# Performance work log

Measured on AMD Instinct MI355X. Metric: run time of the kernel, lower is better.

The kernel has to match this reference:

```python
import jax, jax.numpy as jnp
import numpy as np

N = 20000      # nodes
E = 320000     # edges (avg in-degree 16)
R = 100        # relation types
F = 256        # in_ent_feats == out_ent_feats == in_rel_feats
H = 8          # heads
D = F // H     # head dim = 32
HOP = 5        # PPR hops
ALPHA = 0.1
SLOPE = 0.2    # LeakyReLU negative slope


def _ln(x, g, b, eps=1e-5):
    m = x.mean(-1, keepdims=True)
    v = ((x - m) ** 2).mean(-1, keepdims=True)
    return (x - m) / jnp.sqrt(v + eps) * g + b


def setup_inputs() -> dict:
    key = jax.random.key(0)
    ks = jax.random.split(key, 12)
    s = 1.0 / np.sqrt(F)
    ent_feat = jax.random.normal(ks[0], (N, F), jnp.float32)
    rel_feat = jax.random.normal(ks[1], (R, F), jnp.float32)
    W_head = jax.random.normal(ks[2], (F, F), jnp.float32) * s
    W_tail = jax.random.normal(ks[3], (F, F), jnp.float32) * s
    W_ent = jax.random.normal(ks[4], (F, F), jnp.float32) * s
    W_rel = jax.random.normal(ks[5], (F, F), jnp.float32) * s
    attn = jax.random.normal(ks[6], (1, H, D), jnp.float32) * s
    ln_ent_g = jnp.ones((F,), jnp.float32); ln_ent_b = jnp.zeros((F,), jnp.float32)
    ln_rel_g = jnp.ones((F,), jnp.float32); ln_rel_b = jnp.zeros((F,), jnp.float32)
    ln_ff_g = jnp.ones((F,), jnp.float32); ln_ff_b = jnp.zeros((F,), jnp.float32)
    W1 = jax.random.normal(ks[7], (F, 4 * F), jnp.float32) * s
    b1 = jnp.zeros((4 * F,), jnp.float32)
    W2 = jax.random.normal(ks[8], (4 * F, F), jnp.float32) * (0.5 * s)
    b2 = jnp.zeros((F,), jnp.float32)
    src = jax.random.randint(ks[9], (E,), 0, N, dtype=jnp.int32)
    # every node must have in-degree >= 1 (DGL raises on 0-in-degree nodes)
    dst = jnp.concatenate([jnp.arange(N, dtype=jnp.int32),
                           jax.random.randint(ks[10], (E - N,), 0, N, dtype=jnp.int32)])
    rid = jax.random.randint(ks[11], (E,), 0, R, dtype=jnp.int32)
    return {"ent_feat": ent_feat, "rel_feat": rel_feat,
            "W_head": W_head, "W_tail": W_tail, "W_ent": W_ent, "W_rel": W_rel,
            "attn": attn,
            "ln_ent_g": ln_ent_g, "ln_ent_b": ln_ent_b,
            "ln_rel_g": ln_rel_g, "ln_rel_b": ln_rel_b,
            "ln_ff_g": ln_ff_g, "ln_ff_b": ln_ff_b,
            "W1": W1, "b1": b1, "W2": W2, "b2": b2,
            "src": src, "dst": dst, "rid": rid}


def reference(ent_feat, rel_feat, W_head, W_tail, W_ent, W_rel, attn,
              ln_ent_g, ln_ent_b, ln_rel_g, ln_rel_b, ln_ff_g, ln_ff_b,
              W1, b1, W2, b2, src, dst, rid):
    n = ent_feat.shape[0]
    x = _ln(ent_feat, ln_ent_g, ln_ent_b)                 # [N,F]
    fh = (x @ W_head).reshape(n, H, D)                    # 'eh'
    ftl = (x @ W_tail).reshape(n, H, D)                   # 'et'
    fen = (x @ W_ent).reshape(n, H, D)                    # 'ft'
    r = _ln(rel_feat, ln_rel_g, ln_rel_b)
    fr = (r @ W_rel).reshape(-1, H, D)[rid]               # [E,H,D]
    # relational edge attention score
    e = jax.nn.leaky_relu(fh[src] * ftl[dst] * fr, SLOPE)
    e = (e * attn).sum(-1)                                # [E,H]
    # e_mul_v with log in-degree, scaled by head_dim
    deg = jax.ops.segment_sum(jnp.ones((src.shape[0],), e.dtype), dst, num_segments=n)
    e = e * (jnp.log(deg)[dst])[:, None] / D
    # edge softmax over incoming edges of each dst node, per head
    m = jax.lax.stop_gradient(jax.ops.segment_max(e, dst, num_segments=n))
    ex = jnp.exp(e - m[dst])
    denom = jax.ops.segment_sum(ex, dst, num_segments=n)
    a = ex / denom[dst]                                   # [E,H]
    # PPR-style diffusion aggregation
    feat0 = fen
    feat = fen
    for _ in range(HOP):
        msg = feat[src] * a[:, :, None]                   # [E,H,D]
        agg = jax.ops.segment_sum(msg, dst, num_segments=n)
        feat = (1.0 - ALPHA) * agg + ALPHA * feat0
    # residual (Identity since in_ent_feats == out_ent_feats)
    rst = feat + ent_feat.reshape(n, H, D)
    rst = rst.reshape(n, F)
    # position-wise feed-forward with pre-LN and residual
    y = _ln(rst, ln_ff_g, ln_ff_b)
    ff = jax.nn.relu(y @ W1 + b1) @ W2 + b2
    return ff + rst
```

## Files before the change

kernel.cpp:

```cpp
#include <hip/hip_runtime.h>

#define N_NODES 20000
#define N_EDGES 320000
#define N_REL   100
#define FDIM    256
#define NHEAD   8
#define HDIM    32
#define SCAN_BLOCKS ((N_NODES + 255) / 256)

using short8 = __attribute__((ext_vector_type(8))) short;
using f32x4  = __attribute__((ext_vector_type(4))) float;

__device__ inline unsigned short f2bf(float f) {
    union { float f; unsigned int u; } v; v.f = f;
    unsigned int r = v.u + 0x7fff + ((v.u >> 16) & 1);
    return (unsigned short)(r >> 16);
}
__device__ inline float bf2f(unsigned short u) {
    union { unsigned int i; float f; } v; v.i = ((unsigned int)u) << 16; return v.f;
}
__device__ inline float4 bf4(ushort4 u) {
    return make_float4(bf2f(u.x), bf2f(u.y), bf2f(u.z), bf2f(u.w));
}
__device__ inline void unpack8(float* d, uint4 u) {
    union { unsigned int u; float f; } t;
    t.u = u.x << 16;         d[0] = t.f;
    t.u = u.x & 0xffff0000u; d[1] = t.f;
    t.u = u.y << 16;         d[2] = t.f;
    t.u = u.y & 0xffff0000u; d[3] = t.f;
    t.u = u.z << 16;         d[4] = t.f;
    t.u = u.z & 0xffff0000u; d[5] = t.f;
    t.u = u.w << 16;         d[6] = t.f;
    t.u = u.w & 0xffff0000u; d[7] = t.f;
}
__device__ inline void fma8(float* acc, uint4 u, float w) {
    union { unsigned int u; float f; } t;
    t.u = u.x << 16;         acc[0] += w * t.f;
    t.u = u.x & 0xffff0000u; acc[1] += w * t.f;
    t.u = u.y << 16;         acc[2] += w * t.f;
    t.u = u.y & 0xffff0000u; acc[3] += w * t.f;
    t.u = u.z << 16;         acc[4] += w * t.f;
    t.u = u.z & 0xffff0000u; acc[5] += w * t.f;
    t.u = u.w << 16;         acc[6] += w * t.f;
    t.u = u.w & 0xffff0000u; acc[7] += w * t.f;
}
__device__ __forceinline__ void g2lds16(const unsigned short* g, unsigned short* l) {
    __builtin_amdgcn_global_load_lds(
        (const __attribute__((address_space(1))) unsigned int*)g,
        (__attribute__((address_space(3))) unsigned int*)l,
        16, 0, 0);
}

__global__ __launch_bounds__(64) void ln_bf16_kernel(
    const float* __restrict__ in, const float* __restrict__ g,
    const float* __restrict__ b, unsigned short* __restrict__ out, int rows)
{
    int row = blockIdx.x;
    if (row >= rows) return;
    int tid = threadIdx.x;
    const float4 v = *(const float4*)(in + (size_t)row * FDIM + tid * 4);
    float s = v.x + v.y + v.z + v.w;
    float q = v.x * v.x + v.y * v.y + v.z * v.z + v.w * v.w;
    #pragma unroll
    for (int d = 1; d < 64; d <<= 1) { s += __shfl_xor(s, d); q += __shfl_xor(q, d); }
    float mean = s * (1.0f / FDIM);
    float var  = q * (1.0f / FDIM) - mean * mean;
    float inv  = rsqrtf(var + 1e-5f);
    float4 gg = *(const float4*)(g + tid * 4);
    float4 bb = *(const float4*)(b + tid * 4);
    ushort4 o;
    o.x = f2bf((v.x - mean) * inv * gg.x + bb.x);
    o.y = f2bf((v.y - mean) * inv * gg.y + bb.y);
    o.z = f2bf((v.z - mean) * inv * gg.z + bb.z);
    o.w = f2bf((v.w - mean) * inv * gg.w + bb.w);
    *(ushort4*)(out + (size_t)row * FDIM + tid * 4) = o;
}

__global__ __launch_bounds__(64) void rst_ln_kernel(
    const unsigned short* __restrict__ feat, const float* __restrict__ ent,
    const float* __restrict__ g, const float* __restrict__ b,
    float* __restrict__ rst, unsigned short* __restrict__ y)
{
    int row = blockIdx.x;
    int tid = threadIdx.x;
    const float4 f = bf4(*(const ushort4*)(feat + (size_t)row * FDIM + tid * 4));
    const float4 e = *(const float4*)(ent + (size_t)row * FDIM + tid * 4);
    float4 r;
    r.x = f.x + e.x; r.y = f.y + e.y; r.z = f.z + e.z; r.w = f.w + e.w;
    *(float4*)(rst + (size_t)row * FDIM + tid * 4) = r;
    float s = r.x + r.y + r.z + r.w;
    float q = r.x * r.x + r.y * r.y + r.z * r.z + r.w * r.w;
    #pragma unroll
    for (int d = 1; d < 64; d <<= 1) { s += __shfl_xor(s, d); q += __shfl_xor(q, d); }
    float mean = s * (1.0f / FDIM);
    float var  = q * (1.0f / FDIM) - mean * mean;
    float inv  = rsqrtf(var + 1e-5f);
    float4 gg = *(const float4*)(g + tid * 4);
    float4 bb = *(const float4*)(b + tid * 4);
    ushort4 o;
    o.x = f2bf((r.x - mean) * inv * gg.x + bb.x);
    o.y = f2bf((r.y - mean) * inv * gg.y + bb.y);
    o.z = f2bf((r.z - mean) * inv * gg.z + bb.z);
    o.w = f2bf((r.w - mean) * inv * gg.w + bb.w);
    *(ushort4*)(y + (size_t)row * FDIM + tid * 4) = o;
}

__global__ void transpose_bf16_kernel(const float* __restrict__ W,
                                      unsigned short* __restrict__ Wt, int K, int N)
{
    int idx = blockIdx.x * 256 + threadIdx.x;
    if (idx >= K * N) return;
    int n = idx / K, k = idx - n * K;
    Wt[idx] = f2bf(W[(size_t)k * N + n]);
}

__global__ __launch_bounds__(256) void mfma_gemm_bt(
    const unsigned short* __restrict__ A, const unsigned short* __restrict__ Bt,
    const float* __restrict__ bias, const float* __restrict__ add,
    float* __restrict__ Cf, unsigned short* __restrict__ Cb,
    int M, int K, int N, int relu)
{
    __shared__ unsigned short As[128 * 32];
    __shared__ unsigned short Bs[128 * 32];
    int tid  = threadIdx.x;
    int wave = tid >> 6, lane = tid & 63;
    int quad = lane >> 4, l16 = lane & 15;
    int m0 = blockIdx.x * 128, n0 = blockIdx.y * 128;
    int wr = (wave >> 1) * 64, wc = (wave & 1) * 64;

    f32x4 acc[4][4] = {};

    int cA = tid, cB = tid + 256;
    int rA0 = cA >> 2, kA0 = (cA & 3) * 8;
    int rB0 = cB >> 2, kB0 = (cB & 3) * 8;
    int rA = m0 + rA0; if (rA >= M) rA = M - 1;
    int rB = m0 + rB0; if (rB >= M) rB = M - 1;
    const unsigned short* gA0 = A + (size_t)rA * K + kA0;
    const unsigned short* gA1 = A + (size_t)rB * K + kB0;
    const unsigned short* gB0 = Bt + (size_t)(n0 + rA0) * K + kA0;
    const unsigned short* gB1 = Bt + (size_t)(n0 + rB0) * K + kB0;

    for (int k0 = 0; k0 < K; k0 += 32) {
        g2lds16(gA0 + k0, As + cA * 8);
        g2lds16(gA1 + k0, As + cB * 8);
        g2lds16(gB0 + k0, Bs + cA * 8);
        g2lds16(gB1 + k0, Bs + cB * 8);
        __syncthreads();
        short8 af[4], bfr[4];
        #pragma unroll
        for (int i = 0; i < 4; ++i)
            af[i] = *(const short8*)(As + (wr + i * 16 + l16) * 32 + quad * 8);
        #pragma unroll
        for (int j = 0; j < 4; ++j)
            bfr[j] = *(const short8*)(Bs + (wc + j * 16 + l16) * 32 + quad * 8);
        #pragma unroll
        for (int i = 0; i < 4; ++i)
            #pragma unroll
            for (int j = 0; j < 4; ++j)
                acc[i][j] = __builtin_amdgcn_mfma_f32_16x16x32_bf16(
                    af[i], bfr[j], acc[i][j], 0, 0, 0);
        __syncthreads();
    }

    #pragma unroll
    for (int i = 0; i < 4; ++i) {
        #pragma unroll
        for (int j = 0; j < 4; ++j) {
            int col = n0 + wc + j * 16 + l16;
            float bsv = bias ? bias[col] : 0.0f;
            #pragma unroll
            for (int r = 0; r < 4; ++r) {
                int row = m0 + wr + i * 16 + quad * 4 + r;
                if (row < M) {
                    float v = acc[i][j][r] + bsv;
                    if (relu) v = fmaxf(v, 0.0f);
                    if (add)  v += add[(size_t)row * N + col];
                    if (Cf) Cf[(size_t)row * N + col] = v;
                    else    Cb[(size_t)row * N + col] = f2bf(v);
                }
            }
        }
    }
}

__global__ __launch_bounds__(256) void mfma_gemm64_bt(
    const unsigned short* __restrict__ A, const unsigned short* __restrict__ Bt,
    const float* __restrict__ bias, const float* __restrict__ add,
    float* __restrict__ Cf, int M, int K, int N)
{
    __shared__ unsigned short As[64 * 32];
    __shared__ unsigned short Bs[128 * 32];
    int tid  = threadIdx.x;
    int wave = tid >> 6, lane = tid & 63;
    int quad = lane >> 4, l16 = lane & 15;
    int m0 = blockIdx.x * 64, n0 = blockIdx.y * 128;
    int wc = wave * 32;

    f32x4 acc[4][2] = {};

    int rA0 = tid >> 2, kA0 = (tid & 3) * 8;
    int cB0 = tid, cB1 = tid + 256;
    int rB0 = cB0 >> 2, kB0 = (cB0 & 3) * 8;
    int rB1 = cB1 >> 2, kB1 = (cB1 & 3) * 8;
    int rA = m0 + rA0; if (rA >= M) rA = M - 1;
    const unsigned short* gA  = A + (size_t)rA * K + kA0;
    const unsigned short* gB0 = Bt + (size_t)(n0 + rB0) * K + kB0;
    const unsigned short* gB1 = Bt + (size_t)(n0 + rB1) * K + kB1;

    for (int k0 = 0; k0 < K; k0 += 32) {
        g2lds16(gA + k0,  As + tid * 8);
        g2lds16(gB0 + k0, Bs + cB0 * 8);
        g2lds16(gB1 + k0, Bs + cB1 * 8);
        __syncthreads();
        short8 af[4], bfr[2];
        #pragma unroll
        for (int i = 0; i < 4; ++i)
            af[i] = *(const short8*)(As + (i * 16 + l16) * 32 + quad * 8);
        #pragma unroll
        for (int j = 0; j < 2; ++j)
            bfr[j] = *(const short8*)(Bs + (wc + j * 16 + l16) * 32 + quad * 8);
        #pragma unroll
        for (int i = 0; i < 4; ++i)
            #pragma unroll
            for (int j = 0; j < 2; ++j)
                acc[i][j] = __builtin_amdgcn_mfma_f32_16x16x32_bf16(
                    af[i], bfr[j], acc[i][j], 0, 0, 0);
        __syncthreads();
    }

    #pragma unroll
    for (int i = 0; i < 4; ++i) {
        #pragma unroll
        for (int j = 0; j < 2; ++j) {
            int col = n0 + wc + j * 16 + l16;
            float bsv = bias ? bias[col] : 0.0f;
            #pragma unroll
            for (int r = 0; r < 4; ++r) {
                int row = m0 + i * 16 + quad * 4 + r;
                if (row < M) {
                    float v = acc[i][j][r] + bsv;
                    if (add) v += add[(size_t)row * N + col];
                    Cf[(size_t)row * N + col] = v;
                }
            }
        }
    }
}

__global__ void count_kernel(const int* __restrict__ dst, int* __restrict__ deg, int E)
{
    int i = blockIdx.x * blockDim.x + threadIdx.x;
    if (i < E) atomicAdd(&deg[dst[i]], 1);
}

__global__ __launch_bounds__(256) void scan1_kernel(
    const int* __restrict__ deg, int* __restrict__ offsets, int* __restrict__ bsum, int n)
{
    __shared__ int tmp[256];
    int tid = threadIdx.x;
    int i = blockIdx.x * 256 + tid;
    int v = (i < n) ? deg[i] : 0;
    tmp[tid] = v;
    __syncthreads();
    for (int d = 1; d < 256; d <<= 1) {
        int u = (tid >= d) ? tmp[tid - d] : 0;
        __syncthreads();
        tmp[tid] += u;
        __syncthreads();
    }
    if (i < n) offsets[i] = tmp[tid] - v;
    if (tid == 255) bsum[blockIdx.x] = tmp[255];
}

__global__ __launch_bounds__(128) void scan2_kernel(int* __restrict__ bsum, int nb)
{
    __shared__ int tmp[128];
    int tid = threadIdx.x;
    int v = (tid < nb) ? bsum[tid] : 0;
    tmp[tid] = v;
    __syncthreads();
    for (int d = 1; d < 128; d <<= 1) {
        int u = (tid >= d) ? tmp[tid - d] : 0;
        __syncthreads();
        tmp[tid] += u;
        __syncthreads();
    }
    if (tid < nb) bsum[tid] = tmp[tid] - v;
}

__global__ __launch_bounds__(256) void scan3_kernel(
    const int* __restrict__ deg, int* __restrict__ offsets,
    const int* __restrict__ bsum, int* __restrict__ cursor,
    float* __restrict__ logdeg, int n, int E)
{
    int i = blockIdx.x * 256 + threadIdx.x;
    if (i < n) {
        int o = offsets[i] + bsum[blockIdx.x];
        offsets[i] = o;
        cursor[i]  = o;
        logdeg[i]  = logf((float)deg[i]);
    }
    if (i == 0) offsets[n] = E;
}

__global__ void scatter_kernel(const int* __restrict__ dst, const int* __restrict__ src,
                               const int* __restrict__ rid, int* __restrict__ cursor,
                               int* __restrict__ csr_src, int* __restrict__ csr_rid, int E)
{
    int i = blockIdx.x * blockDim.x + threadIdx.x;
    if (i < E) {
        int p = atomicAdd(&cursor[dst[i]], 1);
        csr_src[p] = src[i];
        csr_rid[p] = rid[i];
    }
}

__global__ __launch_bounds__(256) void edge_score_csr_kernel(
    const unsigned short* __restrict__ proj,
    const unsigned short* __restrict__ frel,
    const float* __restrict__ attn,
    const int* __restrict__ csr_src, const int* __restrict__ csr_rid,
    const int* __restrict__ offsets, const float* __restrict__ logdeg,
    float* __restrict__ csr_a, int n)
{
    int node = blockIdx.x * 4 + (threadIdx.x >> 6);
    if (node >= n) return;
    int tid = threadIdx.x & 63;
    int g = tid >> 4, li = tid & 15;
    int start = offsets[node], end = offsets[node + 1];
    float scale = logdeg[node] * (1.0f / 32.0f);

    float tv[16], at[16];
    {
        const unsigned short* tp = proj + (size_t)node * 768 + 256 + li * 16;
        uint4 a0 = *(const uint4*)tp, a1 = *(const uint4*)(tp + 8);
        unpack8(tv, a0); unpack8(tv + 8, a1);
        const float4* ap = (const float4*)(attn + li * 16);
        float4 f;
        f = ap[0]; at[0] = f.x; at[1] = f.y; at[2]  = f.z; at[3]  = f.w;
        f = ap[1]; at[4] = f.x; at[5] = f.y; at[6]  = f.z; at[7]  = f.w;
        f = ap[2]; at[8] = f.x; at[9] = f.y; at[10] = f.z; at[11] = f.w;
        f = ap[3]; at[12] = f.x; at[13] = f.y; at[14] = f.z; at[15] = f.w;
    }

    float denom = 0.f;
    for (int p = start; p < end; p += 8) {
        int  pe[2]; bool va[2]; uint4 h0[2], h1[2], r0[2], r1[2];
        #pragma unroll
        for (int t = 0; t < 2; ++t) {
            pe[t] = p + t * 4 + g;
            va[t] = pe[t] < end;
            int q = va[t] ? pe[t] : end - 1;
            int s = csr_src[q], r = csr_rid[q];
            const unsigned short* hp = proj + (size_t)s * 768 + li * 16;
            const unsigned short* rp = frel + (size_t)r * FDIM + li * 16;
            h0[t] = *(const uint4*)hp; h1[t] = *(const uint4*)(hp + 8);
            r0[t] = *(const uint4*)rp; r1[t] = *(const uint4*)(rp + 8);
        }
        #pragma unroll
        for (int t = 0; t < 2; ++t) {
            float hv[16], rv[16];
            unpack8(hv, h0[t]); unpack8(hv + 8, h1[t]);
            unpack8(rv, r0[t]); unpack8(rv + 8, r1[t]);
            float sum = 0.f;
            #pragma unroll
            for (int k = 0; k < 16; ++k) {
                float m = hv[k] * tv[k] * rv[k];
                m = (m > 0.f) ? m : 0.2f * m;
                sum += m * at[k];
            }
            sum += __shfl_xor(sum, 1);
            float ex = expf(sum * scale);
            if (va[t] && ((li & 1) == 0)) {
                csr_a[(size_t)pe[t] * NHEAD + (li >> 1)] = ex;
                denom += ex;
            }
        }
    }
    denom += __shfl_xor(denom, 16);
    denom += __shfl_xor(denom, 32);
    float dh = __shfl(denom, 2 * (tid & 7));
    for (int i = start * NHEAD + tid; i < end * NHEAD; i += 64)
        csr_a[i] = csr_a[i] / dh;
}

__global__ __launch_bounds__(256) void diffuse_kernel(
    const unsigned short* __restrict__ fin, int fin_stride,
    const unsigned short* __restrict__ feat0,
    const float* __restrict__ a, const int* __restrict__ csr_src,
    const int* __restrict__ offsets, unsigned short* __restrict__ fout, int n)
{
    int node = blockIdx.x * 4 + (threadIdx.x >> 6);
    if (node >= n) return;
    int tid = threadIdx.x & 63;
    int g = tid >> 4, li = tid & 15;
    int hh = li >> 1;
    int start = offsets[node], end = offsets[node + 1];
    float acc[16] = {};

    for (int p = start; p < end; p += 16) {
        uint4 u0[4], u1[4]; float w[4];
        #pragma unroll
        for (int t = 0; t < 4; ++t) {
            int pe = p + t * 4 + g;
            int q = (pe < end) ? pe : end - 1;
            int s = csr_src[q];
            w[t] = (pe < end) ? a[(size_t)q * NHEAD + hh] : 0.0f;
            const unsigned short* rp = fin + (size_t)s * fin_stride + li * 16;
            u0[t] = *(const uint4*)(rp);
            u1[t] = *(const uint4*)(rp + 8);
        }
        #pragma unroll
        for (int t = 0; t < 4; ++t) {
            fma8(acc + 0, u0[t], w[t]);
            fma8(acc + 8, u1[t], w[t]);
        }
    }
    #pragma unroll
    for (int k = 0; k < 16; ++k) {
        acc[k] += __shfl_xor(acc[k], 16);
        acc[k] += __shfl_xor(acc[k], 32);
    }
    if (g == 0) {
        const unsigned short* f0p = feat0 + (size_t)node * 768 + li * 16;
        uint4 f0a = *(const uint4*)(f0p);
        uint4 f0b = *(const uint4*)(f0p + 8);
        float f0[16];
        unpack8(f0, f0a); unpack8(f0 + 8, f0b);
        unsigned short o[16];
        #pragma unroll
        for (int k = 0; k < 16; ++k) o[k] = f2bf(0.9f * acc[k] + 0.1f * f0[k]);
        uint4* dst4 = (uint4*)(fout + (size_t)node * FDIM + li * 16);
        dst4[0] = *(uint4*)(o);
        dst4[1] = *(uint4*)(o + 8);
    }
}

extern "C" void kernel_launch(void* const* d_in, const int* in_sizes, int n_in,
                              void* d_out, int out_size, void* d_ws, size_t ws_size,
                              hipStream_t stream)
{
    const float* ent_feat = (const float*)d_in[0];
    const float* rel_feat = (const float*)d_in[1];
    const float* W_head   = (const float*)d_in[2];
    const float* W_tail   = (const float*)d_in[3];
    const float* W_ent    = (const float*)d_in[4];
    const float* W_rel    = (const float*)d_in[5];
    const float* attn     = (const float*)d_in[6];
    const float* ln_ent_g = (const float*)d_in[7];
    const float* ln_ent_b = (const float*)d_in[8];
    const float* ln_rel_g = (const float*)d_in[9];
    const float* ln_rel_b = (const float*)d_in[10];
    const float* ln_ff_g  = (const float*)d_in[11];
    const float* ln_ff_b  = (const float*)d_in[12];
    const float* W1       = (const float*)d_in[13];
    const float* b1       = (const float*)d_in[14];
    const float* W2       = (const float*)d_in[15];
    const float* b2       = (const float*)d_in[16];
    const int*   src      = (const int*)d_in[17];
    const int*   dst      = (const int*)d_in[18];
    const int*   rid      = (const int*)d_in[19];
    float* out = (float*)d_out;

    char* base = (char*)d_ws;
    auto carve = [&](size_t bytes) { char* p = base; base += (bytes + 255) & ~(size_t)255; return p; };
    unsigned short* xb    = (unsigned short*)carve((size_t)N_NODES * FDIM * 2);
    unsigned short* projb = (unsigned short*)carve((size_t)N_NODES * 768 * 2);
    unsigned short* rlnb  = (unsigned short*)carve((size_t)N_REL * FDIM * 2);
    unsigned short* frelb = (unsigned short*)carve((size_t)N_REL * FDIM * 2);
    unsigned short* WtP   = (unsigned short*)carve((size_t)768 * FDIM * 2);
    unsigned short* WtR   = (unsigned short*)carve((size_t)FDIM * FDIM * 2);
    unsigned short* W1t   = (unsigned short*)carve((size_t)1024 * FDIM * 2);
    unsigned short* W2t   = (unsigned short*)carve((size_t)FDIM * 1024 * 2);
    unsigned short* hb0   = (unsigned short*)carve((size_t)N_NODES * FDIM * 2);
    unsigned short* hb1   = (unsigned short*)carve((size_t)N_NODES * FDIM * 2);
    unsigned short* yb    = (unsigned short*)carve((size_t)N_NODES * FDIM * 2);
    unsigned short* t1b   = (unsigned short*)carve((size_t)N_NODES * 1024 * 2);
    float* rst     = (float*)carve((size_t)N_NODES * FDIM * 4);
    float* csr_a   = (float*)carve(((size_t)N_EDGES * NHEAD + 256) * 4);
    int*   csr_src = (int*)carve((size_t)(N_EDGES + 64) * 4);
    int*   csr_rid = (int*)carve((size_t)(N_EDGES + 64) * 4);
    int*   deg     = (int*)carve((size_t)N_NODES * 4);
    float* logdeg  = (float*)carve((size_t)N_NODES * 4);
    int*   offsets = (int*)carve((size_t)(N_NODES + 1) * 4);
    int*   cursor  = (int*)carve((size_t)N_NODES * 4);
    int*   bsum    = (int*)carve((size_t)SCAN_BLOCKS * 4);

    hipMemsetAsync(deg, 0, (size_t)N_NODES * 4, stream);

    ln_bf16_kernel<<<N_NODES, 64, 0, stream>>>(ent_feat, ln_ent_g, ln_ent_b, xb, N_NODES);
    ln_bf16_kernel<<<N_REL, 64, 0, stream>>>(rel_feat, ln_rel_g, ln_rel_b, rlnb, N_REL);

    transpose_bf16_kernel<<<(65536 + 255) / 256, 256, 0, stream>>>(W_head, WtP,              FDIM, FDIM);
    transpose_bf16_kernel<<<(65536 + 255) / 256, 256, 0, stream>>>(W_tail, WtP + 256 * FDIM, FDIM, FDIM);
    transpose_bf16_kernel<<<(65536 + 255) / 256, 256, 0, stream>>>(W_ent,  WtP + 512 * FDIM, FDIM, FDIM);
    transpose_bf16_kernel<<<(65536 + 255) / 256, 256, 0, stream>>>(W_rel,  WtR, FDIM, FDIM);
    transpose_bf16_kernel<<<(262144 + 255) / 256, 256, 0, stream>>>(W1, W1t, FDIM, 1024);
    transpose_bf16_kernel<<<(262144 + 255) / 256, 256, 0, stream>>>(W2, W2t, 1024, FDIM);

    dim3 gproj((N_NODES + 127) / 128, 768 / 128);
    mfma_gemm_bt<<<gproj, 256, 0, stream>>>(xb, WtP, nullptr, nullptr, nullptr, projb,
                                            N_NODES, FDIM, 768, 0);
    dim3 grel(1, FDIM / 128);
    mfma_gemm_bt<<<grel, 256, 0, stream>>>(rlnb, WtR, nullptr, nullptr, nullptr, frelb,
                                           N_REL, FDIM, FDIM, 0);

    count_kernel<<<(N_EDGES + 255) / 256, 256, 0, stream>>>(dst, deg, N_EDGES);
    scan1_kernel<<<SCAN_BLOCKS, 256, 0, stream>>>(deg, offsets, bsum, N_NODES);
    scan2_kernel<<<1, 128, 0, stream>>>(bsum, SCAN_BLOCKS);
    scan3_kernel<<<SCAN_BLOCKS, 256, 0, stream>>>(deg, offsets, bsum, cursor, logdeg,
                                                  N_NODES, N_EDGES);
    scatter_kernel<<<(N_EDGES + 255) / 256, 256, 0, stream>>>(dst, src, rid, cursor,
                                                              csr_src, csr_rid, N_EDGES);

    edge_score_csr_kernel<<<(N_NODES + 3) / 4, 256, 0, stream>>>(
        projb, frelb, attn, csr_src, csr_rid, offsets, logdeg, csr_a, N_NODES);

    const unsigned short* fen = projb + 512;
    int gdif = (N_NODES + 3) / 4;
    diffuse_kernel<<<gdif, 256, 0, stream>>>(fen, 768, fen, csr_a, csr_src, offsets, hb0, N_NODES);
    diffuse_kernel<<<gdif, 256, 0, stream>>>(hb0, FDIM, fen, csr_a, csr_src, offsets, hb1, N_NODES);
    diffuse_kernel<<<gdif, 256, 0, stream>>>(hb1, FDIM, fen, csr_a, csr_src, offsets, hb0, N_NODES);
    diffuse_kernel<<<gdif, 256, 0, stream>>>(hb0, FDIM, fen, csr_a, csr_src, offsets, hb1, N_NODES);
    diffuse_kernel<<<gdif, 256, 0, stream>>>(hb1, FDIM, fen, csr_a, csr_src, offsets, hb0, N_NODES);

    rst_ln_kernel<<<N_NODES, 64, 0, stream>>>(hb0, ent_feat, ln_ff_g, ln_ff_b, rst, yb);

    dim3 gff1((N_NODES + 127) / 128, 1024 / 128);
    mfma_gemm_bt<<<gff1, 256, 0, stream>>>(yb, W1t, b1, nullptr, nullptr, t1b,
                                           N_NODES, FDIM, 1024, 1);
    dim3 gff2((N_NODES + 63) / 64, FDIM / 128);
    mfma_gemm64_bt<<<gff2, 256, 0, stream>>>(t1b, W2t, b2, rst, out,
                                             N_NODES, 1024, FDIM);
}
```

Measured before the change: 508.0 us.

## Double-buffer GEMM LDS tiles and remap workgroups across XCDs

Both MFMA GEMM kernels now use two LDS buffers, issuing the global-to-LDS loads for the next K slice before running MFMAs on the current one, so load latency can overlap compute. Workgroup IDs are also remapped so that consecutive tiles land on the same XCD, which is meant to improve L2 reuse of shared A and B rows. The cost is doubled LDS per block, which may lower occupancy. Correctness depends on the async LDS loads having completed by the end-of-iteration barrier.

```diff
diff --git a/kernel.cpp b/kernel.cpp
--- a/kernel.cpp
+++ b/kernel.cpp
@@ -49,6 +49,19 @@
         (const __attribute__((address_space(1))) unsigned int*)g,
         (__attribute__((address_space(3))) unsigned int*)l,
         16, 0, 0);
+}
+
+__device__ inline void xcd_tile(int* m0, int* n0, int tm, int tn) {
+    int nwg  = gridDim.x * gridDim.y;
+    int wgid = blockIdx.x + blockIdx.y * gridDim.x;
+    int q = nwg >> 3, r = nwg & 7;
+    int xcd = wgid & 7, pos = wgid >> 3;
+    int nid = (xcd < r ? xcd * (q + 1) : r * (q + 1) + (xcd - r) * q) + pos;
+    int gy = gridDim.y;
+    int bx = nid / gy;
+    int by = nid - bx * gy;
+    *m0 = bx * tm;
+    *n0 = by * tn;
 }
 
 __global__ __launch_bounds__(64) void ln_bf16_kernel(
@@ -120,12 +133,13 @@
     float* __restrict__ Cf, unsigned short* __restrict__ Cb,
     int M, int K, int N, int relu)
 {
-    __shared__ unsigned short As[128 * 32];
-    __shared__ unsigned short Bs[128 * 32];
+    __shared__ unsigned short As[2][128 * 32];
+    __shared__ unsigned short Bs[2][128 * 32];
     int tid  = threadIdx.x;
     int wave = tid >> 6, lane = tid & 63;
     int quad = lane >> 4, l16 = lane & 15;
-    int m0 = blockIdx.x * 128, n0 = blockIdx.y * 128;
+    int m0, n0;
+    xcd_tile(&m0, &n0, 128, 128);
     int wr = (wave >> 1) * 64, wc = (wave & 1) * 64;
 
     f32x4 acc[4][4] = {};
@@ -140,19 +154,29 @@
     const unsigned short* gB0 = Bt + (size_t)(n0 + rA0) * K + kA0;
     const unsigned short* gB1 = Bt + (size_t)(n0 + rB0) * K + kB0;
 
+    g2lds16(gA0, As[0] + cA * 8);
+    g2lds16(gA1, As[0] + cB * 8);
+    g2lds16(gB0, Bs[0] + cA * 8);
+    g2lds16(gB1, Bs[0] + cB * 8);
+    __syncthreads();
+
+    int cur = 0;
     for (int k0 = 0; k0 < K; k0 += 32) {
-        g2lds16(gA0 + k0, As + cA * 8);
-        g2lds16(gA1 + k0, As + cB * 8);
-        g2lds16(gB0 + k0, Bs + cA * 8);
-        g2lds16(gB1 + k0, Bs + cB * 8);
-        __syncthreads();
+        int k1 = k0 + 32;
+        if (k1 < K) {
+            int nb = cur ^ 1;
+            g2lds16(gA0 + k1, As[nb] + cA * 8);
+            g2lds16(gA1 + k1, As[nb] + cB * 8);
+            g2lds16(gB0 + k1, Bs[nb] + cA * 8);
+            g2lds16(gB1 + k1, Bs[nb] + cB * 8);
+        }
         short8 af[4], bfr[4];
         #pragma unroll
         for (int i = 0; i < 4; ++i)
-            af[i] = *(const short8*)(As + (wr + i * 16 + l16) * 32 + quad * 8);
+            af[i] = *(const short8*)(As[cur] + (wr + i * 16 + l16) * 32 + quad * 8);
         #pragma unroll
         for (int j = 0; j < 4; ++j)
-            bfr[j] = *(const short8*)(Bs + (wc + j * 16 + l16) * 32 + quad * 8);
+            bfr[j] = *(const short8*)(Bs[cur] + (wc + j * 16 + l16) * 32 + quad * 8);
         #pragma unroll
         for (int i = 0; i < 4; ++i)
             #pragma unroll
@@ -160,6 +184,7 @@
                 acc[i][j] = __builtin_amdgcn_mfma_f32_16x16x32_bf16(
                     af[i], bfr[j], acc[i][j], 0, 0, 0);
         __syncthreads();
+        cur ^= 1;
     }
 
     #pragma unroll
@@ -188,12 +213,13 @@
     const float* __restrict__ bias, const float* __restrict__ add,
     float* __restrict__ Cf, int M, int K, int N)
 {
-    __shared__ unsigned short As[64 * 32];
-    __shared__ unsigned short Bs[128 * 32];
+    __shared__ unsigned short As[2][64 * 32];
+    __shared__ unsigned short Bs[2][128 * 32];
     int tid  = threadIdx.x;
     int wave = tid >> 6, lane = tid & 63;
     int quad = lane >> 4, l16 = lane & 15;
-    int m0 = blockIdx.x * 64, n0 = blockIdx.y * 128;
+    int m0, n0;
+    xcd_tile(&m0, &n0, 64, 128);
     int wc = wave * 32;
 
     f32x4 acc[4][2] = {};
@@ -207,18 +233,27 @@
     const unsigned short* gB0 = Bt + (size_t)(n0 + rB0) * K + kB0;
     const unsigned short* gB1 = Bt + (size_t)(n0 + rB1) * K + kB1;
 
+    g2lds16(gA,  As[0] + tid * 8);
+    g2lds16(gB0, Bs[0] + cB0 * 8);
+    g2lds16(gB1, Bs[0] + cB1 * 8);
+    __syncthreads();
+
+    int cur = 0;
     for (int k0 = 0; k0 < K; k0 += 32) {
-        g2lds16(gA + k0,  As + tid * 8);
-        g2lds16(gB0 + k0, Bs + cB0 * 8);
-        g2lds16(gB1 + k0, Bs + cB1 * 8);
-        __syncthreads();
+        int k1 = k0 + 32;
+        if (k1 < K) {
+            int nb = cur ^ 1;
+            g2lds16(gA + k1,  As[nb] + tid * 8);
+            g2lds16(gB0 + k1, Bs[nb] + cB0 * 8);
+            g2lds16(gB1 + k1, Bs[nb] + cB1 * 8);
+        }
         short8 af[4], bfr[2];
         #pragma unroll
         for (int i = 0; i < 4; ++i)
-            af[i] = *(const short8*)(As + (i * 16 + l16) * 32 + quad * 8);
+            af[i] = *(const short8*)(As[cur] + (i * 16 + l16) * 32 + quad * 8);
         #pragma unroll
         for (int j = 0; j < 2; ++j)
-            bfr[j] = *(const short8*)(Bs + (wc + j * 16 + l16) * 32 + quad * 8);
+            bfr[j] = *(const short8*)(Bs[cur] + (wc + j * 16 + l16) * 32 + quad * 8);
         #pragma unroll
         for (int i = 0; i < 4; ++i)
             #pragma unroll
@@ -226,6 +261,7 @@
                 acc[i][j] = __builtin_amdgcn_mfma_f32_16x16x32_bf16(
                     af[i], bfr[j], acc[i][j], 0, 0, 0);
         __syncthreads();
+        cur ^= 1;
     }
 
     #pragma unroll
```

Result: faster. 495.0 us (-2.6%).
